# Performance work log

Hardware: AMD Instinct MI355X
Metric: run time of the kernel (lower is better)

## Reference

```python
import math
import jax, jax.numpy as jnp
import numpy as np

N_EXPERTS = 8
N_ACTIVE = 5
N_CAMP_A = 4
TEMPERATURE = math.e


def setup_inputs() -> dict:
    key = jax.random.key(0)
    ks = jax.random.split(key, 5)
    B, T, D, I = 4, 2048, 2048, 1024
    s = 0.02
    return {
        "x": jax.random.normal(ks[0], (B, T, D), jnp.float32),
        "Wr": jax.random.normal(ks[1], (D, N_EXPERTS), jnp.float32) * s,
        "Wg": jax.random.normal(ks[2], (N_EXPERTS, D, I), jnp.float32) * s,
        "Wu": jax.random.normal(ks[3], (N_EXPERTS, D, I), jnp.float32) * s,
        "Wd": jax.random.normal(ks[4], (N_EXPERTS, I, D), jnp.float32) * s,
    }


def _router_weights(x, Wr):
    # scores: (B,T,E)
    probs = jax.nn.softmax(jnp.einsum("btd,de->bte", x, Wr) / TEMPERATURE, axis=-1)
    _, topk_idx = jax.lax.top_k(probs, N_ACTIVE)          # (B,T,k)
    mask = jax.nn.one_hot(topk_idx, N_EXPERTS, dtype=probs.dtype).sum(axis=-2)
    w = probs * mask
    return w / (w.sum(axis=-1, keepdims=True) + 1e-8)


def reference(x, Wr, Wg, Wu, Wd):
    weights = _router_weights(x, Wr)                       # (B,T,E)
    # All experts run on full dense input (faithful to source loop), batched GEMMs.
    g = jnp.einsum("btd,edi->btei", x, Wg)                 # (B,T,E,I)
    u = jnp.einsum("btd,edi->btei", x, Wu)
    h = jax.nn.silu(g) * u
    eo = jnp.einsum("btei,eid->bted", h, Wd)               # (B,T,E,D)
    sign = jnp.concatenate([jnp.ones(N_CAMP_A), -jnp.ones(N_EXPERTS - N_CAMP_A)]).astype(x.dtype)
    output = jnp.einsum("bte,bted->btd", weights * sign, eo)  # out_a - out_g
    tension_scalar = jax.lax.stop_gradient(jnp.mean(output ** 2))
    return output, tension_scalar
```

## Files before the change

### kernel.cpp

```cpp
#include <hip/hip_runtime.h>
#include <cstdint>
#include <cstddef>


typedef short bf16x8 __attribute__((ext_vector_type(8)));
typedef float f32x4 __attribute__((ext_vector_type(4)));
typedef unsigned short u16;

typedef const unsigned int __attribute__((address_space(1)))* as1_u32p;
typedef unsigned int __attribute__((address_space(3)))* as3_u32p;

#define VMCNT6 asm volatile("s_waitcnt vmcnt(6)" ::: "memory")
#define VMCNT0 asm volatile("s_waitcnt vmcnt(0)" ::: "memory")
#define LGKM0  asm volatile("s_waitcnt lgkmcnt(0)" ::: "memory")
#define LGKM8  asm volatile("s_waitcnt lgkmcnt(8)" ::: "memory")
#define SBAR   __builtin_amdgcn_s_barrier()
#define SCHED0 __builtin_amdgcn_sched_barrier(0)
#define PRIO1  __builtin_amdgcn_s_setprio(1)
#define PRIO0  __builtin_amdgcn_s_setprio(0)
#define MFMA16(af, bf, cf) __builtin_amdgcn_mfma_f32_16x16x32_bf16(af, bf, cf, 0, 0, 0)

__device__ __forceinline__ u16 f2bf(float f) {
  unsigned u = __builtin_bit_cast(unsigned, f);
  u += 0x7fffu + ((u >> 16) & 1u);
  return (u16)(u >> 16);
}

__device__ __forceinline__ void gload16(const void* g, const u16* lds) {
  as1_u32p gp = (as1_u32p)(uintptr_t)g;
  as3_u32p lp = (as3_u32p)(unsigned)(uintptr_t)lds;
  __builtin_amdgcn_global_load_lds(gp, lp, 16, 0, 0);
}

__global__ __launch_bounds__(256) void router_kernel(
    const float* __restrict__ x, const float* __restrict__ Wr,
    float* __restrict__ Cw, u16* __restrict__ Xb) {
  const int l = threadIdx.x & 63;
  const int t = blockIdx.x * 4 + (threadIdx.x >> 6);
  const float* xr = x + (size_t)t * 2048;
  u16* xbr = Xb + (size_t)t * 2048;
  float p[8] = {0.f,0.f,0.f,0.f,0.f,0.f,0.f,0.f};
#pragma unroll
  for (int it = 0; it < 8; ++it) {
    const int d0 = it * 256 + l * 4;
    const float4 xv = *(const float4*)(xr + d0);
    unsigned lo = (unsigned)f2bf(xv.x) | ((unsigned)f2bf(xv.y) << 16);
    unsigned hi = (unsigned)f2bf(xv.z) | ((unsigned)f2bf(xv.w) << 16);
    *(unsigned*)(xbr + d0) = lo;
    *(unsigned*)(xbr + d0 + 2) = hi;
    const float xs[4] = {xv.x, xv.y, xv.z, xv.w};
#pragma unroll
    for (int jj = 0; jj < 4; ++jj) {
      const float4 w0 = *(const float4*)(Wr + (size_t)(d0 + jj) * 8);
      const float4 w1 = *(const float4*)(Wr + (size_t)(d0 + jj) * 8 + 4);
      p[0] += xs[jj] * w0.x; p[1] += xs[jj] * w0.y;
      p[2] += xs[jj] * w0.z; p[3] += xs[jj] * w0.w;
      p[4] += xs[jj] * w1.x; p[5] += xs[jj] * w1.y;
      p[6] += xs[jj] * w1.z; p[7] += xs[jj] * w1.w;
    }
  }
#pragma unroll
  for (int e = 0; e < 8; ++e) {
    float v = p[e];
#pragma unroll
    for (int off = 32; off > 0; off >>= 1) v += __shfl_xor(v, off, 64);
    p[e] = v;
  }
  constexpr float INV_TEMP = 0.36787944117144233f;
  float mx = -1e30f;
#pragma unroll
  for (int e = 0; e < 8; ++e) { p[e] *= INV_TEMP; mx = fmaxf(mx, p[e]); }
  float sum = 0.f;
#pragma unroll
  for (int e = 0; e < 8; ++e) { p[e] = __expf(p[e] - mx); sum += p[e]; }
  const float inv_sum = 1.f / sum;
#pragma unroll
  for (int e = 0; e < 8; ++e) p[e] *= inv_sum;
  unsigned sel = 0xFFu;
  for (int it = 0; it < 3; ++it) {
    float mn = 1e30f; int mi = 0;
#pragma unroll
    for (int e = 0; e < 8; ++e)
      if ((sel >> e) & 1u) { if (p[e] <= mn) { mn = p[e]; mi = e; } }
    sel &= ~(1u << mi);
  }
  float wsum = 0.f;
#pragma unroll
  for (int e = 0; e < 8; ++e) if ((sel >> e) & 1u) wsum += p[e];
  const float inv_w = 1.f / (wsum + 1e-8f);
  if (l == 0) {
#pragma unroll
    for (int e = 0; e < 8; ++e) {
      float v = ((sel >> e) & 1u) ? p[e] * inv_w : 0.f;
      Cw[(size_t)t * 8 + e] = (e < 4) ? v : -v;
    }
  }
}

__global__ __launch_bounds__(256) void build_idx(
    const float* __restrict__ Cw, int* __restrict__ idx, int* __restrict__ cnt) {
  const int e = blockIdx.x;
  const int tid = threadIdx.x;
  const int t0 = tid * 32;
  int c = 0;
#pragma unroll
  for (int j = 0; j < 32; ++j)
    if (Cw[(size_t)(t0 + j) * 8 + e] != 0.f) ++c;
  __shared__ int s[256];
  s[tid] = c;
  __syncthreads();
  for (int off = 1; off < 256; off <<= 1) {
    int v = (tid >= off) ? s[tid - off] : 0;
    __syncthreads();
    s[tid] += v;
    __syncthreads();
  }
  int o = e * 8192 + s[tid] - c;
  for (int j = 0; j < 32; ++j) {
    const int t = t0 + j;
    if (Cw[(size_t)t * 8 + e] != 0.f) idx[o++] = t;
  }
  if (tid == 255) cnt[e] = s[255];
}

__global__ __launch_bounds__(256) void zerofill(
    const float* __restrict__ Cw, u16* __restrict__ Hp, int p) {
  const int t = blockIdx.x * 4 + (threadIdx.x >> 6);
  const int l = threadIdx.x & 63;
  bf16x8* rowp = (bf16x8*)(Hp + (size_t)t * 4096);
  const bf16x8 z = {0, 0, 0, 0, 0, 0, 0, 0};
#pragma unroll
  for (int el = 0; el < 4; ++el) {
    if (Cw[(size_t)t * 8 + p * 4 + el] == 0.f) {
      rowp[el * 128 + l] = z;
      rowp[el * 128 + 64 + l] = z;
    }
  }
}

__global__ __launch_bounds__(256) void tcvt_kernel(
    const float* __restrict__ in, u16* __restrict__ out,
    int R, int C, long long ZO, long long CS) {
  __shared__ float tile[64][65];
  const int z = blockIdx.z;
  const float* ib = in + (size_t)z * R * C;
  const int r0 = blockIdx.y * 64, c0 = blockIdx.x * 64;
  const int tx = threadIdx.x, ty = threadIdx.y;
#pragma unroll
  for (int j = 0; j < 16; ++j)
    tile[ty + j * 4][tx] = ib[(size_t)(r0 + ty + j * 4) * C + c0 + tx];
  __syncthreads();
#pragma unroll
  for (int j = 0; j < 16; ++j)
    out[(size_t)z * ZO + (size_t)(c0 + ty + j * 4) * CS + r0 + tx] =
        f2bf(tile[tx][ty + j * 4]);
}


__global__ __launch_bounds__(512, 2) void gemm1_8p(
    const u16* __restrict__ Xb, const u16* __restrict__ Wgt,
    const u16* __restrict__ Wut, const float* __restrict__ Cw,
    u16* __restrict__ Hp, const int* __restrict__ idx,
    const int* __restrict__ cnt, int p) {
  extern __shared__ u16 lds[];
  const int tid = threadIdx.x;
  const int l = tid & 63, w = tid >> 6;
  const int wr = w >> 2, wc = w & 3;
  const int lq = l >> 4, lr = l & 15;
  const int bid = blockIdx.x;
  const int work = (bid & 7) * 128 + (bid >> 3);
  const int mtile = work & 31;
  const int en = work >> 5;
  const int el = en >> 3, nt = en & 7;
  const int e = p * 4 + el;
  const int cnt_e = idx ? cnt[e] : 8192;
  const int base = mtile * 256;
  if (base >= cnt_e) return;
  const int* idxp = idx ? idx + (size_t)e * 8192 : nullptr;

  const u16* s0p = Wgt + (size_t)e * 2097152 + (size_t)nt * 128 * 2048;
  const u16* s1p = Wut + (size_t)e * 2097152 + (size_t)nt * 128 * 2048;

  const int lrow = tid >> 3;
  const int cgo = ((tid & 7) ^ (lrow & 7)) * 8;
  const int offB0 = lrow * 2048 + cgo;
  const int offB1 = offB0 + 64 * 2048;
  const int d0e = tid * 8, d1e = (512 + tid) * 8;

  auto gr = [&](int r) -> size_t {
    const int rr = r < cnt_e ? r : cnt_e - 1;
    return (size_t)(idxp ? idxp[rr] : rr) * 2048 + cgo;
  };
  const size_t a20 = gr(base + lrow);
  const size_t a21 = gr(base + 64 + lrow);
  const size_t a30 = gr(base + 128 + lrow);
  const size_t a31 = gr(base + 192 + lrow);

  const int NT = 32;
  auto stageB = [&](int tt, const u16* srcb, int u) {
    if (tt >= NT) return;
    u16* dst = lds + (tt & 1) * 32768 + u * 8192;
    const int kt = tt * 64;
    gload16(srcb + offB0 + kt, dst + d0e);
    gload16(srcb + offB1 + kt, dst + d1e);
  };
  auto stageA = [&](int tt, size_t b0, size_t b1, int u) {
    if (tt >= NT) return;
    u16* dst = lds + (tt & 1) * 32768 + u * 8192;
    const int kt = tt * 64;
    gload16(Xb + b0 + kt, dst + d0e);
    gload16(Xb + b1 + kt, dst + d1e);
  };

  const int xr = lr & 7;
  const int x0 = (lq ^ xr) * 8;
  const int x1 = ((4 + lq) ^ xr) * 8;
  const int aB = (2 + wr) * 8192 + lr * 64;
  const int gBo = (wc * 32 + lr) * 64;
  const int uBo = 8192 + (wc * 32 + lr) * 64;

  bf16x8 a[8][2], bg[2][2], bu[2][2];
  f32x4 ag[8][2], au[8][2];
#pragma unroll
  for (int mi = 0; mi < 8; ++mi)
#pragma unroll
    for (int ni = 0; ni < 2; ++ni) {
      ag[mi][ni] = (f32x4){0.f, 0.f, 0.f, 0.f};
      au[mi][ni] = (f32x4){0.f, 0.f, 0.f, 0.f};
    }

  stageB(0, s0p, 0); stageB(0, s1p, 1);
  stageA(0, a20, a21, 2); stageA(0, a30, a31, 3);
  stageB(1, s0p, 0); stageB(1, s1p, 1); stageA(1, a20, a21, 2);
  VMCNT6; SBAR;

  for (int t = 0; t < NT; ++t) {
    const u16* Lb = lds + (t & 1) * 32768;
    {
#pragma unroll
      for (int mi = 0; mi < 4; ++mi) {
        a[mi][0] = *(const bf16x8*)&Lb[aB + mi * 1024 + x0];
        a[mi][1] = *(const bf16x8*)&Lb[aB + mi * 1024 + x1];
      }
#pragma unroll
      for (int ni = 0; ni < 2; ++ni) {
        bg[ni][0] = *(const bf16x8*)&Lb[gBo + ni * 1024 + x0];
        bg[ni][1] = *(const bf16x8*)&Lb[gBo + ni * 1024 + x1];
      }
      stageA(t + 1, a30, a31, 3);
      LGKM8; SBAR; LGKM0; SCHED0;
      PRIO1;
#pragma unroll
      for (int mi = 0; mi < 4; ++mi)
#pragma unroll
        for (int ni = 0; ni < 2; ++ni)
#pragma unroll
          for (int kk = 0; kk < 2; ++kk)
            ag[mi][ni] = MFMA16(a[mi][kk], bg[ni][kk], ag[mi][ni]);
      PRIO0; SCHED0; SBAR;
    }
    {
#pragma unroll
      for (int ni = 0; ni < 2; ++ni) {
        bu[ni][0] = *(const bf16x8*)&Lb[uBo + ni * 1024 + x0];
        bu[ni][1] = *(const bf16x8*)&Lb[uBo + ni * 1024 + x1];
      }
      stageB(t + 2, s0p, 0);
      SBAR; LGKM0; SCHED0;
      PRIO1;
#pragma unroll
      for (int mi = 0; mi < 4; ++mi)
#pragma unroll
        for (int ni = 0; ni < 2; ++ni)
#pragma unroll
          for (int kk = 0; kk < 2; ++kk)
            au[mi][ni] = MFMA16(a[mi][kk], bu[ni][kk], au[mi][ni]);
      PRIO0; SCHED0; SBAR;
    }
    {
#pragma unroll
      for (int mi = 4; mi < 8; ++mi) {
        a[mi][0] = *(const bf16x8*)&Lb[aB + mi * 1024 + x0];
        a[mi][1] = *(const bf16x8*)&Lb[aB + mi * 1024 + x1];
      }
      stageB(t + 2, s1p, 1);
      SBAR; LGKM0; SCHED0;
      PRIO1;
#pragma unroll
      for (int mi = 4; mi < 8; ++mi)
#pragma unroll
        for (int ni = 0; ni < 2; ++ni)
#pragma unroll
          for (int kk = 0; kk < 2; ++kk)
            ag[mi][ni] = MFMA16(a[mi][kk], bg[ni][kk], ag[mi][ni]);
      PRIO0; SCHED0; SBAR;
    }
    {
      stageA(t + 2, a20, a21, 2);
      if (t < NT - 2) { VMCNT6; } else if (t == NT - 2) { VMCNT0; }
      SBAR; LGKM0; SCHED0;
      PRIO1;
#pragma unroll
      for (int mi = 4; mi < 8; ++mi)
#pragma unroll
        for (int ni = 0; ni < 2; ++ni)
#pragma unroll
          for (int kk = 0; kk < 2; ++kk)
            au[mi][ni] = MFMA16(a[mi][kk], bu[ni][kk], au[mi][ni]);
      PRIO0; SCHED0; SBAR;
    }
  }

#pragma unroll
  for (int mi = 0; mi < 8; ++mi) {
#pragma unroll
    for (int j = 0; j < 4; ++j) {
      const int rl = wr * 128 + mi * 16 + lq * 4 + j;
      const int grow = base + rl;
      if (grow < cnt_e) {
        const int orow = idxp ? idxp[grow] : grow;
        const float c = Cw[(size_t)orow * 8 + e];
#pragma unroll
        for (int ni = 0; ni < 2; ++ni) {
          const float g = ag[mi][ni][j], u = au[mi][ni][j];
          const float h = g * (1.f / (1.f + __expf(-g))) * u * c;
          Hp[(size_t)orow * 4096 + el * 1024 + nt * 128 + wc * 32 + ni * 16 + lr] =
              f2bf(h);
        }
      }
    }
  }
}

__global__ __launch_bounds__(512, 2) void gemm2_8p(
    const u16* __restrict__ Hp, const u16* __restrict__ Wdt,
    float* __restrict__ out, float* __restrict__ part, int koff, int accum) {
  extern __shared__ u16 lds[];
  const int tid = threadIdx.x;
  const int l = tid & 63, w = tid >> 6;
  const int wr = w >> 2, wc = w & 3;
  const int lq = l >> 4, lr = l & 15;
  const int bid = blockIdx.x;
  const int work = (bid & 7) * 32 + (bid >> 3);
  const int mtile = work & 31, ntile = work >> 5;
  const u16* gA = Hp + (size_t)mtile * 256 * 4096;
  const u16* gB = Wdt + (size_t)ntile * 256 * 8192 + koff;
  const u16* s0p = gB;
  const u16* s1p = gB + (size_t)128 * 8192;
  const u16* s2p = gA;
  const u16* s3p = gA + (size_t)128 * 4096;
  const int NT = 64;

  const int row0 = tid >> 3,          cg0 = (tid & 7) ^ (row0 & 7);
  const int row1 = (512 + tid) >> 3,  cg1 = ((512 + tid) & 7) ^ (row1 & 7);
  const int offA0 = row0 * 4096 + cg0 * 8, offA1 = row1 * 4096 + cg1 * 8;
  const int offB0 = row0 * 8192 + cg0 * 8, offB1 = row1 * 8192 + cg1 * 8;
  const int d0e = tid * 8, d1e = (512 + tid) * 8;

  auto stageA = [&](int tt, const u16* srcb, int u) {
    if (tt >= NT) return;
    u16* dst = lds + (tt & 1) * 32768 + u * 8192;
    const int kt = tt * 64;
    gload16(srcb + (size_t)(offA0 + kt), dst + d0e);
    gload16(srcb + (size_t)(offA1 + kt), dst + d1e);
  };
  auto stageB = [&](int tt, const u16* srcb, int u) {
    if (tt >= NT) return;
    u16* dst = lds + (tt & 1) * 32768 + u * 8192;
    const int kt = tt * 64;
    gload16(srcb + (size_t)(offB0 + kt), dst + d0e);
    gload16(srcb + (size_t)(offB1 + kt), dst + d1e);
  };

  const int xr = lr & 7;
  const int x0 = (lq ^ xr) * 8;
  const int x1 = ((4 + lq) ^ xr) * 8;
  const int aB = (2 + wr) * 8192 + lr * 64;
  const int bB = (wc >> 1) * 8192 + ((wc & 1) * 64 + lr) * 64;

  bf16x8 a[8][2], b[4][2];
  f32x4 acc[8][4];
#pragma unroll
  for (int mi = 0; mi < 8; ++mi)
#pragma unroll
    for (int ni = 0; ni < 4; ++ni) acc[mi][ni] = (f32x4){0.f, 0.f, 0.f, 0.f};

  stageB(0, s0p, 0); stageB(0, s1p, 1); stageA(0, s2p, 2); stageA(0, s3p, 3);
  stageB(1, s0p, 0); stageB(1, s1p, 1); stageA(1, s2p, 2);
  VMCNT6; SBAR;

  for (int t = 0; t < NT; ++t) {
    const u16* Lb = lds + (t & 1) * 32768;
    {
#pragma unroll
      for (int mi = 0; mi < 4; ++mi) {
        a[mi][0] = *(const bf16x8*)&Lb[aB + mi * 1024 + x0];
        a[mi][1] = *(const bf16x8*)&Lb[aB + mi * 1024 + x1];
      }
#pragma unroll
      for (int ni = 0; ni < 2; ++ni) {
        b[ni][0] = *(const bf16x8*)&Lb[bB + ni * 1024 + x0];
        b[ni][1] = *(const bf16x8*)&Lb[bB + ni * 1024 + x1];
      }
      if (wc < 2) {
#pragma unroll
        for (int ni = 2; ni < 4; ++ni) {
          b[ni][0] = *(const bf16x8*)&Lb[bB + ni * 1024 + x0];
          b[ni][1] = *(const bf16x8*)&Lb[bB + ni * 1024 + x1];
        }
      }
      stageA(t + 1, s3p, 3);
      LGKM8; SBAR; LGKM0; SCHED0;
      PRIO1;
#pragma unroll
      for (int mi = 0; mi < 4; ++mi)
#pragma unroll
        for (int ni = 0; ni < 2; ++ni)
#pragma unroll
          for (int kk = 0; kk < 2; ++kk)
            acc[mi][ni] = MFMA16(a[mi][kk], b[ni][kk], acc[mi][ni]);
      PRIO0; SCHED0; SBAR;
    }
    {
      if (wc >= 2) {
#pragma unroll
        for (int ni = 2; ni < 4; ++ni) {
          b[ni][0] = *(const bf16x8*)&Lb[bB + ni * 1024 + x0];
          b[ni][1] = *(const bf16x8*)&Lb[bB + ni * 1024 + x1];
        }
      }
      stageB(t + 2, s0p, 0);
      SBAR; LGKM0; SCHED0;
      PRIO1;
#pragma unroll
      for (int mi = 0; mi < 4; ++mi)
#pragma unroll
        for (int ni = 2; ni < 4; ++ni)
#pragma unroll
          for (int kk = 0; kk < 2; ++kk)
            acc[mi][ni] = MFMA16(a[mi][kk], b[ni][kk], acc[mi][ni]);
      PRIO0; SCHED0; SBAR;
    }
    {
#pragma unroll
      for (int mi = 4; mi < 8; ++mi) {
        a[mi][0] = *(const bf16x8*)&Lb[aB + mi * 1024 + x0];
        a[mi][1] = *(const bf16x8*)&Lb[aB + mi * 1024 + x1];
      }
      stageB(t + 2, s1p, 1);
      SBAR; LGKM0; SCHED0;
      PRIO1;
#pragma unroll
      for (int mi = 4; mi < 8; ++mi)
#pragma unroll
        for (int ni = 2; ni < 4; ++ni)
#pragma unroll
          for (int kk = 0; kk < 2; ++kk)
            acc[mi][ni] = MFMA16(a[mi][kk], b[ni][kk], acc[mi][ni]);
      PRIO0; SCHED0; SBAR;
    }
    {
      stageA(t + 2, s2p, 2);
      if (t < NT - 2) { VMCNT6; } else if (t == NT - 2) { VMCNT0; }
      SBAR; LGKM0; SCHED0;
      PRIO1;
#pragma unroll
      for (int mi = 4; mi < 8; ++mi)
#pragma unroll
        for (int ni = 0; ni < 2; ++ni)
#pragma unroll
          for (int kk = 0; kk < 2; ++kk)
            acc[mi][ni] = MFMA16(a[mi][kk], b[ni][kk], acc[mi][ni]);
      PRIO0; SCHED0; SBAR;
    }
  }

  float sq = 0.f;
#pragma unroll
  for (int mi = 0; mi < 8; ++mi)
#pragma unroll
    for (int ni = 0; ni < 4; ++ni)
#pragma unroll
      for (int j = 0; j < 4; ++j) {
        const int row = mtile * 256 + wr * 128 + mi * 16 + lq * 4 + j;
        const int col = ntile * 256 + wc * 64 + ni * 16 + lr;
        const size_t idx2 = (size_t)row * 2048 + col;
        float v = acc[mi][ni][j];
        if (accum) { v += out[idx2]; sq += v * v; }
        out[idx2] = v;
      }
  if (accum) {
#pragma unroll
    for (int off = 32; off > 0; off >>= 1) sq += __shfl_down(sq, off, 64);
    __syncthreads();
    float* sm = (float*)lds;
    if (l == 0) sm[w] = sq;
    __syncthreads();
    if (tid == 0) {
      float tot = 0.f;
#pragma unroll
      for (int i = 0; i < 8; ++i) tot += sm[i];
      part[bid] = tot;
    }
  }
}

__global__ __launch_bounds__(256) void sqsum_final(
    const float* __restrict__ part, float* __restrict__ dst, int np, float scale) {
  float s = 0.f;
  for (int i = threadIdx.x; i < np; i += 256) s += part[i];
#pragma unroll
  for (int off = 32; off > 0; off >>= 1) s += __shfl_down(s, off, 64);
  __shared__ float ls[4];
  if ((threadIdx.x & 63) == 0) ls[threadIdx.x >> 6] = s;
  __syncthreads();
  if (threadIdx.x == 0) dst[0] = (ls[0] + ls[1] + ls[2] + ls[3]) * scale;
}

extern "C" void kernel_launch(void* const* d_in, const int* in_sizes, int n_in,
                              void* d_out, int out_size, void* d_ws, size_t ws_size,
                              hipStream_t stream) {
  (void)in_sizes; (void)n_in; (void)out_size;
  const float* x  = (const float*)d_in[0];
  const float* Wr = (const float*)d_in[1];
  const float* Wg = (const float*)d_in[2];
  const float* Wu = (const float*)d_in[3];
  const float* Wd = (const float*)d_in[4];
  float* out = (float*)d_out;
  char* ws = (char*)d_ws;
  u16*   Xb   = (u16*)(ws);
  u16*   Wgt  = (u16*)(ws + 33554432);
  u16*   Wut  = (u16*)(ws + 67108864);
  u16*   Wdt  = (u16*)(ws + 100663296);
  u16*   Hp   = (u16*)(ws + 134217728);
  float* Cw   = (float*)(ws + 201326592);
  float* part = (float*)(ws + 201588736);
  const bool SPARSE = ws_size >= 201855008u;
  int* idxbuf = SPARSE ? (int*)(ws + 201592832) : nullptr;
  int* cntbuf = SPARSE ? (int*)(ws + 201854976) : nullptr;

  (void)hipFuncSetAttribute((const void*)gemm1_8p,
                            hipFuncAttributeMaxDynamicSharedMemorySize, 131072);
  (void)hipFuncSetAttribute((const void*)gemm2_8p,
                            hipFuncAttributeMaxDynamicSharedMemorySize, 131072);

  router_kernel<<<2048, 256, 0, stream>>>(x, Wr, Cw, Xb);
  if (SPARSE) build_idx<<<8, 256, 0, stream>>>(Cw, idxbuf, cntbuf);

  dim3 tb(64, 4);
  tcvt_kernel<<<dim3(16, 32, 8), tb, 0, stream>>>(Wg, Wgt, 2048, 1024, 2097152LL, 2048LL);
  tcvt_kernel<<<dim3(16, 32, 8), tb, 0, stream>>>(Wu, Wut, 2048, 1024, 2097152LL, 2048LL);
  tcvt_kernel<<<dim3(32, 16, 8), tb, 0, stream>>>(Wd, Wdt, 1024, 2048, 1024LL, 8192LL);

  for (int p = 0; p < 2; ++p) {
    if (SPARSE) zerofill<<<2048, 256, 0, stream>>>(Cw, Hp, p);
    gemm1_8p<<<1024, 512, 131072, stream>>>(Xb, Wgt, Wut, Cw, Hp,
                                            idxbuf, cntbuf, p);
    gemm2_8p<<<256, 512, 131072, stream>>>(Hp, Wdt, out, part, p * 4096, p);
  }

  sqsum_final<<<1, 256, 0, stream>>>(part, out + 16777216, 256, 1.f / 16777216.f);
}
```

Before: 806.4 us.

## Prefetch next-iteration B fragments in GEMM loops and merge weight transpose kernels

```diff
diff --git a/kernel.cpp b/kernel.cpp
--- a/kernel.cpp
+++ b/kernel.cpp
@@ -13,7 +13,7 @@
 #define VMCNT6 asm volatile("s_waitcnt vmcnt(6)" ::: "memory")
 #define VMCNT0 asm volatile("s_waitcnt vmcnt(0)" ::: "memory")
 #define LGKM0  asm volatile("s_waitcnt lgkmcnt(0)" ::: "memory")
-#define LGKM8  asm volatile("s_waitcnt lgkmcnt(8)" ::: "memory")
+#define LGKM4  asm volatile("s_waitcnt lgkmcnt(4)" ::: "memory")
 #define SBAR   __builtin_amdgcn_s_barrier()
 #define SCHED0 __builtin_amdgcn_sched_barrier(0)
 #define PRIO1  __builtin_amdgcn_s_setprio(1)
@@ -138,13 +138,20 @@
   }
 }
 
-__global__ __launch_bounds__(256) void tcvt_kernel(
-    const float* __restrict__ in, u16* __restrict__ out,
-    int R, int C, long long ZO, long long CS) {
+__global__ __launch_bounds__(256) void tcvt3_kernel(
+    const float* __restrict__ Wg, const float* __restrict__ Wu,
+    const float* __restrict__ Wd, u16* __restrict__ Wgt,
+    u16* __restrict__ Wut, u16* __restrict__ Wdt) {
   __shared__ float tile[64][65];
   const int z = blockIdx.z;
-  const float* ib = in + (size_t)z * R * C;
+  const int which = z >> 3, zs = z & 7;
+  const float* in; u16* out; int R, C; long long ZO, CS;
+  if (which == 0)      { in = Wg; out = Wgt; R = 2048; C = 1024; ZO = 2097152; CS = 2048; }
+  else if (which == 1) { in = Wu; out = Wut; R = 2048; C = 1024; ZO = 2097152; CS = 2048; }
+  else                 { in = Wd; out = Wdt; R = 1024; C = 2048; ZO = 1024;    CS = 8192; }
   const int r0 = blockIdx.y * 64, c0 = blockIdx.x * 64;
+  if (r0 >= R || c0 >= C) return;
+  const float* ib = in + (size_t)zs * R * C;
   const int tx = threadIdx.x, ty = threadIdx.y;
 #pragma unroll
   for (int j = 0; j < 16; ++j)
@@ -152,7 +159,7 @@
   __syncthreads();
 #pragma unroll
   for (int j = 0; j < 16; ++j)
-    out[(size_t)z * ZO + (size_t)(c0 + ty + j * 4) * CS + r0 + tx] =
+    out[(size_t)zs * ZO + (size_t)(c0 + ty + j * 4) * CS + r0 + tx] =
         f2bf(tile[tx][ty + j * 4]);
 }
 
@@ -233,6 +240,11 @@
   stageA(0, a20, a21, 2); stageA(0, a30, a31, 3);
   stageB(1, s0p, 0); stageB(1, s1p, 1); stageA(1, a20, a21, 2);
   VMCNT6; SBAR;
+#pragma unroll
+  for (int ni = 0; ni < 2; ++ni) {
+    bg[ni][0] = *(const bf16x8*)&lds[gBo + ni * 1024 + x0];
+    bg[ni][1] = *(const bf16x8*)&lds[gBo + ni * 1024 + x1];
+  }
 
   for (int t = 0; t < NT; ++t) {
     const u16* Lb = lds + (t & 1) * 32768;
@@ -242,13 +254,8 @@
         a[mi][0] = *(const bf16x8*)&Lb[aB + mi * 1024 + x0];
         a[mi][1] = *(const bf16x8*)&Lb[aB + mi * 1024 + x1];
       }
-#pragma unroll
-      for (int ni = 0; ni < 2; ++ni) {
-        bg[ni][0] = *(const bf16x8*)&Lb[gBo + ni * 1024 + x0];
-        bg[ni][1] = *(const bf16x8*)&Lb[gBo + ni * 1024 + x1];
-      }
       stageA(t + 1, a30, a31, 3);
-      LGKM8; SBAR; LGKM0; SCHED0;
+      LGKM4; SBAR; LGKM0; SCHED0;
       PRIO1;
 #pragma unroll
       for (int mi = 0; mi < 4; ++mi)
@@ -307,7 +314,16 @@
 #pragma unroll
           for (int kk = 0; kk < 2; ++kk)
             au[mi][ni] = MFMA16(a[mi][kk], bu[ni][kk], au[mi][ni]);
-      PRIO0; SCHED0; SBAR;
+      PRIO0; SCHED0;
+      {
+        const u16* Ln = lds + ((t + 1) & 1) * 32768;
+#pragma unroll
+        for (int ni = 0; ni < 2; ++ni) {
+          bg[ni][0] = *(const bf16x8*)&Ln[gBo + ni * 1024 + x0];
+          bg[ni][1] = *(const bf16x8*)&Ln[gBo + ni * 1024 + x1];
+        }
+      }
+      SBAR;
     }
   }
 
@@ -388,6 +404,18 @@
   stageB(0, s0p, 0); stageB(0, s1p, 1); stageA(0, s2p, 2); stageA(0, s3p, 3);
   stageB(1, s0p, 0); stageB(1, s1p, 1); stageA(1, s2p, 2);
   VMCNT6; SBAR;
+#pragma unroll
+  for (int ni = 0; ni < 2; ++ni) {
+    b[ni][0] = *(const bf16x8*)&lds[bB + ni * 1024 + x0];
+    b[ni][1] = *(const bf16x8*)&lds[bB + ni * 1024 + x1];
+  }
+  if (wc < 2) {
+#pragma unroll
+    for (int ni = 2; ni < 4; ++ni) {
+      b[ni][0] = *(const bf16x8*)&lds[bB + ni * 1024 + x0];
+      b[ni][1] = *(const bf16x8*)&lds[bB + ni * 1024 + x1];
+    }
+  }
 
   for (int t = 0; t < NT; ++t) {
     const u16* Lb = lds + (t & 1) * 32768;
@@ -397,38 +425,26 @@
         a[mi][0] = *(const bf16x8*)&Lb[aB + mi * 1024 + x0];
         a[mi][1] = *(const bf16x8*)&Lb[aB + mi * 1024 + x1];
       }
-#pragma unroll
-      for (int ni = 0; ni < 2; ++ni) {
-        b[ni][0] = *(const bf16x8*)&Lb[bB + ni * 1024 + x0];
-        b[ni][1] = *(const bf16x8*)&Lb[bB + ni * 1024 + x1];
-      }
-      if (wc < 2) {
+      stageA(t + 1, s3p, 3);
+      LGKM4; SBAR; LGKM0; SCHED0;
+      PRIO1;
+#pragma unroll
+      for (int mi = 0; mi < 4; ++mi)
+#pragma unroll
+        for (int ni = 0; ni < 2; ++ni)
+#pragma unroll
+          for (int kk = 0; kk < 2; ++kk)
+            acc[mi][ni] = MFMA16(a[mi][kk], b[ni][kk], acc[mi][ni]);
+      PRIO0; SCHED0; SBAR;
+    }
+    {
+      if (wc >= 2) {
 #pragma unroll
         for (int ni = 2; ni < 4; ++ni) {
           b[ni][0] = *(const bf16x8*)&Lb[bB + ni * 1024 + x0];
           b[ni][1] = *(const bf16x8*)&Lb[bB + ni * 1024 + x1];
         }
       }
-      stageA(t + 1, s3p, 3);
-      LGKM8; SBAR; LGKM0; SCHED0;
-      PRIO1;
-#pragma unroll
-      for (int mi = 0; mi < 4; ++mi)
-#pragma unroll
-        for (int ni = 0; ni < 2; ++ni)
-#pragma unroll
-          for (int kk = 0; kk < 2; ++kk)
-            acc[mi][ni] = MFMA16(a[mi][kk], b[ni][kk], acc[mi][ni]);
-      PRIO0; SCHED0; SBAR;
-    }
-    {
-      if (wc >= 2) {
-#pragma unroll
-        for (int ni = 2; ni < 4; ++ni) {
-          b[ni][0] = *(const bf16x8*)&Lb[bB + ni * 1024 + x0];
-          b[ni][1] = *(const bf16x8*)&Lb[bB + ni * 1024 + x1];
-        }
-      }
       stageB(t + 2, s0p, 0);
       SBAR; LGKM0; SCHED0;
       PRIO1;
@@ -471,7 +487,23 @@
 #pragma unroll
           for (int kk = 0; kk < 2; ++kk)
             acc[mi][ni] = MFMA16(a[mi][kk], b[ni][kk], acc[mi][ni]);
-      PRIO0; SCHED0; SBAR;
+      PRIO0; SCHED0;
+      {
+        const u16* Ln = lds + ((t + 1) & 1) * 32768;
+#pragma unroll
+        for (int ni = 0; ni < 2; ++ni) {
+          b[ni][0] = *(const bf16x8*)&Ln[bB + ni * 1024 + x0];
+          b[ni][1] = *(const bf16x8*)&Ln[bB + ni * 1024 + x1];
+        }
+        if (wc < 2) {
+#pragma unroll
+          for (int ni = 2; ni < 4; ++ni) {
+            b[ni][0] = *(const bf16x8*)&Ln[bB + ni * 1024 + x0];
+            b[ni][1] = *(const bf16x8*)&Ln[bB + ni * 1024 + x1];
+          }
+        }
+      }
+      SBAR;
     }
   }
 
@@ -547,10 +579,8 @@
   router_kernel<<<2048, 256, 0, stream>>>(x, Wr, Cw, Xb);
   if (SPARSE) build_idx<<<8, 256, 0, stream>>>(Cw, idxbuf, cntbuf);
 
-  dim3 tb(64, 4);
-  tcvt_kernel<<<dim3(16, 32, 8), tb, 0, stream>>>(Wg, Wgt, 2048, 1024, 2097152LL, 2048LL);
-  tcvt_kernel<<<dim3(16, 32, 8), tb, 0, stream>>>(Wu, Wut, 2048, 1024, 2097152LL, 2048LL);
-  tcvt_kernel<<<dim3(32, 16, 8), tb, 0, stream>>>(Wd, Wdt, 1024, 2048, 1024LL, 8192LL);
+  tcvt3_kernel<<<dim3(32, 32, 24), dim3(64, 4), 0, stream>>>(
+      Wg, Wu, Wd, Wgt, Wut, Wdt);
 
   for (int p = 0; p < 2; ++p) {
     if (SPARSE) zerofill<<<2048, 256, 0, stream>>>(Cw, Hp, p);
```

Result: no change. 806.0 us, median of 2 (-0.1%).
